# Performance work log

Hardware: AMD Instinct MI355X
Metric: run time of the kernel (lower is better)

The kernel has to match this reference:

```python
import jax, jax.numpy as jnp
import numpy as np

B, S, D, O, E = 8, 4096, 1024, 1024, 64

def setup_inputs() -> dict:
    key = jax.random.key(0)
    kx, kgw, kgb, kew, keb = jax.random.split(key, 5)
    x = jax.random.normal(kx, (B, S, D), dtype=jnp.float32)
    gate_w = jax.random.normal(kgw, (E, D), dtype=jnp.float32) * 0.02
    gate_b = jnp.zeros((E,), dtype=jnp.float32)
    expert_w = jax.random.normal(kew, (E, D, O), dtype=jnp.float32) * 0.02
    expert_b = jnp.zeros((E, O), dtype=jnp.float32)
    return {"x": x, "gate_w": gate_w, "gate_b": gate_b,
            "expert_w": expert_w, "expert_b": expert_b}

def reference(x, gate_w, gate_b, expert_w, expert_b):
    # x: [B,S,D] -> flatten tokens. With world_size=1 the all-reduce and
    # all-to-alls in the torch module are identities, and per-chunk processing
    # is token-independent, so one global pass is mathematically identical.
    b, s, d = x.shape
    xt = x.reshape(-1, d)                                   # [N, D]
    logits = xt @ gate_w.T + gate_b                         # [N, E]
    gates = jax.nn.softmax(logits, axis=-1)
    sel = jnp.argmax(gates, axis=-1)                        # [N] top-1 expert
    order = jnp.argsort(sel)                                # stable sort by expert
    xs = xt[order]                                          # tokens grouped by expert
    counts = jnp.bincount(sel, length=E).astype(jnp.int32)  # tokens per expert
    # Grouped expert GEMM: row block e of xs multiplies expert_w[e].
    ys = jax.lax.ragged_dot(xs, expert_w, counts)           # [N, O]
    ys = ys + expert_b[sel[order]]
    # Combine: scatter sorted outputs back to original token positions.
    # (Note: torch output is NOT scaled by gate probability.)
    out = jnp.zeros((xt.shape[0], expert_w.shape[-1]), dtype=ys.dtype)
    out = out.at[order].set(ys)
    return out.reshape(b, s, -1)
```

## Files before the change

kernel.cpp:

```cpp
#include <hip/hip_runtime.h>
#include <hip/hip_bf16.h>

#define N_TOK 32768
#define DIM 1024
#define OUTD 1024
#define NEXP 64

typedef __attribute__((ext_vector_type(4))) float f32x4;
typedef __attribute__((ext_vector_type(8))) short bf16x8;

__device__ __forceinline__ unsigned short f2bf(float f) {
    unsigned int u = __builtin_bit_cast(unsigned int, f);
    u += 0x7FFFu + ((u >> 16) & 1u);
    return (unsigned short)(u >> 16);
}

#define GLOAD16(gp, lp) \
    __builtin_amdgcn_global_load_lds((const __attribute__((address_space(1))) void*)(gp), \
                                     (__attribute__((address_space(3))) void*)(lp), 16, 0, 0)

__global__ __launch_bounds__(256) void prep_kernel(const float* __restrict__ x,
        const float* __restrict__ gw, const float* __restrict__ gb,
        const float* __restrict__ ew,
        int* __restrict__ sel, int* __restrict__ nflag, int* __restrict__ flags,
        int* __restrict__ counts,
        unsigned short* __restrict__ xb, unsigned short* __restrict__ wt)
{
    __shared__ __align__(16) char smem[18688];
    int tid = threadIdx.x;

    if (blockIdx.x < 512) {
        float (*xs)[36]  = (float(*)[36])smem;
        float (*wsm)[36] = (float(*)[36])(smem + 9216);
        int* h = (int*)(smem + 18432);
        if (tid < NEXP) h[tid] = 0;
        int t0 = blockIdx.x * 64;
        int tg = tid >> 4, eg = tid & 15;

        float acc[4][4];
#pragma unroll
        for (int i = 0; i < 4; i++)
#pragma unroll
            for (int j = 0; j < 4; j++) acc[i][j] = 0.f;

        for (int k0 = 0; k0 < DIM; k0 += 32) {
            __syncthreads();
#pragma unroll
            for (int q = 0; q < 2; q++) {
                int cidx = tid + q * 256;
                int r = cidx >> 3, c4 = (cidx & 7) * 4;
                *reinterpret_cast<float4*>(&xs[r][c4]) =
                    *reinterpret_cast<const float4*>(&x[(size_t)(t0 + r) * DIM + k0 + c4]);
                *reinterpret_cast<float4*>(&wsm[r][c4]) =
                    *reinterpret_cast<const float4*>(&gw[(size_t)r * DIM + k0 + c4]);
            }
            __syncthreads();
            if (xb) {
                int r = tid >> 2, cc = (tid & 3) * 8;
                float4 v0 = *reinterpret_cast<const float4*>(&xs[r][cc]);
                float4 v1 = *reinterpret_cast<const float4*>(&xs[r][cc + 4]);
                uint4 p;
                p.x = (unsigned int)f2bf(v0.x) | ((unsigned int)f2bf(v0.y) << 16);
                p.y = (unsigned int)f2bf(v0.z) | ((unsigned int)f2bf(v0.w) << 16);
                p.z = (unsigned int)f2bf(v1.x) | ((unsigned int)f2bf(v1.y) << 16);
                p.w = (unsigned int)f2bf(v1.z) | ((unsigned int)f2bf(v1.w) << 16);
                *reinterpret_cast<uint4*>(&xb[(size_t)(t0 + r) * DIM + k0 + cc]) = p;
            }
#pragma unroll
            for (int kk4 = 0; kk4 < 8; kk4++) {
                float4 xv[4], wv[4];
#pragma unroll
                for (int i = 0; i < 4; i++)
                    xv[i] = *reinterpret_cast<const float4*>(&xs[tg + 16 * i][kk4 * 4]);
#pragma unroll
                for (int j = 0; j < 4; j++)
                    wv[j] = *reinterpret_cast<const float4*>(&wsm[eg + 16 * j][kk4 * 4]);
#pragma unroll
                for (int i = 0; i < 4; i++)
#pragma unroll
                    for (int j = 0; j < 4; j++) {
                        acc[i][j] = fmaf(xv[i].x, wv[j].x, acc[i][j]);
                        acc[i][j] = fmaf(xv[i].y, wv[j].y, acc[i][j]);
                        acc[i][j] = fmaf(xv[i].z, wv[j].z, acc[i][j]);
                        acc[i][j] = fmaf(xv[i].w, wv[j].w, acc[i][j]);
                    }
            }
        }
#pragma unroll
        for (int j = 0; j < 4; j++) {
            float b = gb[eg + 16 * j];
#pragma unroll
            for (int i = 0; i < 4; i++) acc[i][j] += b;
        }
#pragma unroll
        for (int i = 0; i < 4; i++) {
            float m1 = -1e30f, m2 = -1e30f; int e1 = 0;
#pragma unroll
            for (int j = 0; j < 4; j++) {
                float v = acc[i][j]; int e = eg + 16 * j;
                if (v > m1) { m2 = m1; m1 = v; e1 = e; }
                else if (v > m2) m2 = v;
            }
#pragma unroll
            for (int d = 1; d < 16; d <<= 1) {
                float om1 = __shfl_xor(m1, d, 16);
                float om2 = __shfl_xor(m2, d, 16);
                int   oe1 = __shfl_xor(e1, d, 16);
                if (om1 > m1 || (om1 == m1 && oe1 < e1)) {
                    m2 = fmaxf(om2, m1); m1 = om1; e1 = oe1;
                } else {
                    m2 = fmaxf(m2, om1);
                }
            }
            if (eg == 0) {
                int t = t0 + tg + 16 * i;
                sel[t] = e1;
                atomicAdd(&h[e1], 1);
                if (m1 - m2 < 1e-3f) {
                    int idx = atomicAdd(nflag, 1);
                    if (idx < 4096) flags[idx] = t;
                }
            }
        }
        __syncthreads();
        if (tid < NEXP && h[tid]) atomicAdd(&counts[tid], h[tid]);
    } else {
        if (!wt) return;
        unsigned short* ts0 = (unsigned short*)smem;
        unsigned short* ts1 = (unsigned short*)(smem + 9216);
        int lin = blockIdx.x - 512;
        int e = lin >> 5;
        int d0 = ((lin >> 4) & 1) * 512;
        int o0 = (lin & 15) * 64;
        const float* src = ew + (size_t)e * (DIM * OUTD);
        unsigned short* dst = wt + (size_t)e * (DIM * OUTD);
        int og = tid & 7;
        int dl = tid >> 3;
        int dc = tid & 7;
        int ol = tid >> 3;

        float4 c0, c1, c2, c3;
        {
            const float* sr0 = &src[(size_t)(d0 + dl) * OUTD + o0 + og * 8];
            const float* sr1 = &src[(size_t)(d0 + dl + 32) * OUTD + o0 + og * 8];
            c0 = *reinterpret_cast<const float4*>(sr0);
            c1 = *reinterpret_cast<const float4*>(sr0 + 4);
            c2 = *reinterpret_cast<const float4*>(sr1);
            c3 = *reinterpret_cast<const float4*>(sr1 + 4);
        }
#pragma unroll
        for (int s = 0; s < 8; ++s) {
            float4 n0 = c0, n1 = c1, n2 = c2, n3 = c3;
            if (s < 7) {
                int dsn = d0 + (s + 1) * 64;
                const float* sr0 = &src[(size_t)(dsn + dl) * OUTD + o0 + og * 8];
                const float* sr1 = &src[(size_t)(dsn + dl + 32) * OUTD + o0 + og * 8];
                n0 = *reinterpret_cast<const float4*>(sr0);
                n1 = *reinterpret_cast<const float4*>(sr0 + 4);
                n2 = *reinterpret_cast<const float4*>(sr1);
                n3 = *reinterpret_cast<const float4*>(sr1 + 4);
            }
            unsigned short* tsb = (s & 1) ? ts1 : ts0;
#pragma unroll
            for (int half = 0; half < 2; ++half) {
                int dLoc = dl + 32 * half;
                float4 va = half ? c2 : c0;
                float4 vb = half ? c3 : c1;
                unsigned short b[8] = { f2bf(va.x), f2bf(va.y), f2bf(va.z), f2bf(va.w),
                                        f2bf(vb.x), f2bf(vb.y), f2bf(vb.z), f2bf(vb.w) };
                int dg = dLoc >> 3, dr = dLoc & 7;
#pragma unroll
                for (int k = 0; k < 8; k++) {
                    int o = og * 8 + k;
                    int key = (o & 7) ^ ((o >> 3) & 7);
                    tsb[o * 72 + ((dg ^ key) << 3) + dr] = b[k];
                }
            }
            __syncthreads();
            int ds0 = d0 + s * 64;
#pragma unroll
            for (int i = 0; i < 2; i++) {
                int o = ol + 32 * i;
                int key = (o & 7) ^ ((o >> 3) & 7);
                uint4 v = *reinterpret_cast<const uint4*>(&tsb[o * 72 + ((dc ^ key) << 3)]);
                *reinterpret_cast<uint4*>(&dst[(size_t)(o0 + o) * DIM + ds0 + dc * 8]) = v;
            }
            c0 = n0; c1 = n1; c2 = n2; c3 = n3;
        }
    }
}

__global__ __launch_bounds__(64) void gate_fix_kernel(const float* __restrict__ x,
        const float* __restrict__ gw, const float* __restrict__ gb,
        int* __restrict__ sel, const int* __restrict__ nflag, const int* __restrict__ flags,
        int* __restrict__ counts)
{
    int n = *nflag; if (n > 4096) n = 4096;
    int b = blockIdx.x;
    if (b >= n) return;
    int t = flags[b];
    int e = threadIdx.x;
    const float* xr = x + (size_t)t * DIM;
    const float* wr = gw + (size_t)e * DIM;
    double acc = (double)gb[e];
    for (int k = 0; k < DIM; k += 4) {
        acc += (double)xr[k]   * (double)wr[k];
        acc += (double)xr[k+1] * (double)wr[k+1];
        acc += (double)xr[k+2] * (double)wr[k+2];
        acc += (double)xr[k+3] * (double)wr[k+3];
    }
    double m1 = acc; int e1 = e;
#pragma unroll
    for (int d = 1; d < 64; d <<= 1) {
        double om1 = __shfl_xor(m1, d, 64);
        int   oe1  = __shfl_xor(e1, d, 64);
        if (om1 > m1 || (om1 == m1 && oe1 < e1)) { m1 = om1; e1 = oe1; }
    }
    if (e == 0) {
        int eOld = sel[t];
        if (eOld != e1) {
            sel[t] = e1;
            atomicSub(&counts[eOld], 1);
            atomicAdd(&counts[e1], 1);
        }
    }
}

__global__ void sched_kernel(const int* __restrict__ counts, int* __restrict__ offsets,
                             int* __restrict__ schedE, int* __restrict__ schedR,
                             int* __restrict__ totalRB, int rowsShift)
{
    int e = threadIdx.x;
    int c = counts[e];
    int v = c;
#pragma unroll
    for (int d = 1; d < 64; d <<= 1) { int y = __shfl_up(v, d, 64); if (e >= d) v += y; }
    offsets[e] = v - c;
    if (e == 63) offsets[NEXP] = v;
    int rows = 1 << rowsShift;
    int nb = (c + rows - 1) >> rowsShift;
    int rbv = nb;
#pragma unroll
    for (int d = 1; d < 64; d <<= 1) { int y = __shfl_up(rbv, d, 64); if (e >= d) rbv += y; }
    int rbBase = rbv - nb;
    for (int i = 0; i < nb; i++) { schedE[rbBase + i] = e; schedR[rbBase + i] = i << rowsShift; }
    if (e == 63) *totalRB = rbv;
}

__global__ __launch_bounds__(256) void scatter_kernel(const int* __restrict__ sel,
        const int* __restrict__ offsets, int* __restrict__ cursor, int* __restrict__ perm)
{
    int t = blockIdx.x * 256 + threadIdx.x;
    int e = sel[t];
    int pos = offsets[e] + atomicAdd(&cursor[e], 1);
    perm[pos] = t;
}

__global__ __launch_bounds__(512, 4) void moe_gemm7(
        const unsigned short* __restrict__ xb, const unsigned short* __restrict__ wt,
        const float* __restrict__ eb,
        const int* __restrict__ perm, const int* __restrict__ offsets,
        const int* __restrict__ counts, const int* __restrict__ schedE,
        const int* __restrict__ schedR, const int* __restrict__ totalRB,
        float* __restrict__ out)
{
    int idx = blockIdx.x;
    int xcd = idx & 7;
    int s = idx >> 3;
    int cb = s & 7;
    int rb = (s >> 3) * 8 + xcd;
    if (rb >= *totalRB) return;
    int e = schedE[rb], r0 = schedR[rb];
    int cnt = counts[e], base = offsets[e];

    __shared__ __align__(16) unsigned short As[24576];
    __shared__ __align__(16) unsigned short Bs[12288];

    int tid = threadIdx.x;
    int lane = tid & 63;
    int wv = tid >> 6;
    int wr = wv >> 1, wc = wv & 1;
    int lr = lane & 15, lg = lane >> 4;

    int rowS = tid >> 2;
    int koff = ((tid & 3) ^ ((tid >> 3) & 3)) * 8;
    int rA1 = r0 + rowS, rA2 = r0 + 128 + rowS;
    int tokA1 = (rA1 < cnt) ? perm[base + rA1] : 0;
    int tokA2 = (rA2 < cnt) ? perm[base + rA2] : 0;

    const unsigned short* wte = wt + ((size_t)e << 20);
    const unsigned short* aSrc1 = xb + (size_t)tokA1 * DIM + koff;
    const unsigned short* aSrc2 = xb + (size_t)tokA2 * DIM + koff;
    const unsigned short* bSrc1 = wte + (size_t)(cb * 128 + rowS) * DIM + koff;

    unsigned short* AsQ0 = As + wv * 512;
    unsigned short* AsQ1 = As + 4096 + wv * 512;
    unsigned short* BsQ0 = Bs + wv * 512;

    f32x4 acc[4][4];
#pragma unroll
    for (int m = 0; m < 4; m++)
#pragma unroll
        for (int n = 0; n < 4; n++)
#pragma unroll
            for (int c = 0; c < 4; c++) acc[m][n][c] = 0.f;

    const char* Asc = (const char*)As;
    const char* Bsc = (const char*)Bs;
    int fko = (lg ^ ((lr >> 1) & 3)) * 16;

    auto stage = [&](int buf, int k0) {
        GLOAD16(aSrc1 + k0, AsQ0 + buf * 8192);
        GLOAD16(aSrc2 + k0, AsQ1 + buf * 8192);
        GLOAD16(bSrc1 + k0, BsQ0 + buf * 4096);
    };
    auto compute = [&](int buf) {
        int aoff = buf * 16384;
        int boff = buf * 8192;
        bf16x8 bfr[4];
#pragma unroll
        for (int n = 0; n < 4; n++) {
            int row = wc * 64 + n * 16 + lr;
            bfr[n] = *reinterpret_cast<const bf16x8*>(Bsc + boff + (row << 6) + fko);
        }
        __builtin_amdgcn_s_setprio(1);
#pragma unroll
        for (int m = 0; m < 4; m++) {
            int row = wr * 64 + m * 16 + lr;
            bf16x8 afr = *reinterpret_cast<const bf16x8*>(Asc + aoff + (row << 6) + fko);
#pragma unroll
            for (int n = 0; n < 4; n++)
                acc[m][n] = __builtin_amdgcn_mfma_f32_16x16x32_bf16(afr, bfr[n], acc[m][n], 0, 0, 0);
        }
        __builtin_amdgcn_s_setprio(0);
    };

    stage(0, 0);
    stage(1, 32);

    int cbuf = 0, sbuf = 2;
#pragma unroll 1
    for (int t = 0; t < 30; ++t) {
        asm volatile("s_waitcnt vmcnt(3)" ::: "memory");
        __builtin_amdgcn_s_barrier();
        stage(sbuf, (t + 2) * 32);
        compute(cbuf);
        cbuf = (cbuf == 2) ? 0 : cbuf + 1;
        sbuf = (sbuf == 2) ? 0 : sbuf + 1;
    }
    asm volatile("s_waitcnt vmcnt(3)" ::: "memory");
    __builtin_amdgcn_s_barrier();
    compute(cbuf);
    cbuf = (cbuf == 2) ? 0 : cbuf + 1;
    asm volatile("s_waitcnt vmcnt(0)" ::: "memory");
    __builtin_amdgcn_s_barrier();
    compute(cbuf);

    float bias[4];
#pragma unroll
    for (int n = 0; n < 4; n++)
        bias[n] = eb[e * OUTD + cb * 128 + wc * 64 + n * 16 + lr];
#pragma unroll
    for (int m = 0; m < 4; m++) {
        int rowLoc = wr * 64 + m * 16 + lg * 4;
#pragma unroll
        for (int i2 = 0; i2 < 4; i2++) {
            int r = r0 + rowLoc + i2;
            if (r < cnt) {
                int tk = perm[base + r];
#pragma unroll
                for (int n = 0; n < 4; n++) {
                    int oc = cb * 128 + wc * 64 + n * 16 + lr;
                    out[(size_t)tk * OUTD + oc] = acc[m][n][i2] + bias[n];
                }
            }
        }
    }
}

__global__ __launch_bounds__(256) void moe_gemm_legacy(const float* __restrict__ x,
        const float* __restrict__ ew, const float* __restrict__ eb,
        const int* __restrict__ perm, const int* __restrict__ offsets,
        const int* __restrict__ counts, const int* __restrict__ schedE,
        const int* __restrict__ schedR, const int* __restrict__ totalRB,
        float* __restrict__ out)
{
    int rb = blockIdx.x;
    if (rb >= *totalRB) return;
    int cb = blockIdx.y;
    int e = schedE[rb], r0 = schedR[rb];
    int cnt = counts[e], base = offsets[e];

    __shared__ __align__(16) unsigned short As[128][40];
    __shared__ __align__(16) unsigned short Bs[128][40];
    __shared__ int toks[128];

    int tid = threadIdx.x;
    if (tid < 128) {
        int r = r0 + tid;
        toks[tid] = (r < cnt) ? perm[base + r] : -1;
    }
    __syncthreads();

    int lane = tid & 63;
    int wave = tid >> 6;
    int wr = wave >> 1, wc = wave & 1;
    int lr = lane & 15, lg = lane >> 4;

    f32x4 acc[4][4];
#pragma unroll
    for (int m = 0; m < 4; m++)
#pragma unroll
        for (int n = 0; n < 4; n++)
#pragma unroll
            for (int c = 0; c < 4; c++) acc[m][n][c] = 0.f;

    int aRow[4]; int aTok[4];
#pragma unroll
    for (int q = 0; q < 4; q++) {
        aRow[q] = (tid >> 3) + q * 32;
        int tk = toks[aRow[q]];
        aTok[q] = (tk < 0) ? 0 : tk;
    }
    int ac4 = tid & 7;
    int d0 = (tid >> 5) * 4;
    int o_lane = tid & 31;
    const float* wb = ew + (size_t)e * (DIM * OUTD) + (size_t)cb * 128;

    for (int k0 = 0; k0 < DIM; k0 += 32) {
        float4 av[4];
#pragma unroll
        for (int q = 0; q < 4; q++)
            av[q] = *reinterpret_cast<const float4*>(&x[(size_t)aTok[q] * DIM + k0 + ac4 * 4]);
        float bv[4][4];
#pragma unroll
        for (int i2 = 0; i2 < 4; i2++)
#pragma unroll
            for (int j = 0; j < 4; j++)
                bv[i2][j] = wb[(size_t)(k0 + d0 + i2) * OUTD + o_lane + 32 * j];

        __syncthreads();
#pragma unroll
        for (int q = 0; q < 4; q++) {
            uint2 p;
            p.x = (unsigned int)f2bf(av[q].x) | ((unsigned int)f2bf(av[q].y) << 16);
            p.y = (unsigned int)f2bf(av[q].z) | ((unsigned int)f2bf(av[q].w) << 16);
            *reinterpret_cast<uint2*>(&As[aRow[q]][ac4 * 4]) = p;
        }
#pragma unroll
        for (int j = 0; j < 4; j++) {
            uint2 p;
            p.x = (unsigned int)f2bf(bv[0][j]) | ((unsigned int)f2bf(bv[1][j]) << 16);
            p.y = (unsigned int)f2bf(bv[2][j]) | ((unsigned int)f2bf(bv[3][j]) << 16);
            *reinterpret_cast<uint2*>(&Bs[o_lane + 32 * j][d0]) = p;
        }
        __syncthreads();

        bf16x8 bfr[4];
#pragma unroll
        for (int n = 0; n < 4; n++)
            bfr[n] = *reinterpret_cast<const bf16x8*>(&Bs[wc * 64 + n * 16 + lr][lg * 8]);
#pragma unroll
        for (int m = 0; m < 4; m++) {
            bf16x8 afr = *reinterpret_cast<const bf16x8*>(&As[wr * 64 + m * 16 + lr][lg * 8]);
#pragma unroll
            for (int n = 0; n < 4; n++)
                acc[m][n] = __builtin_amdgcn_mfma_f32_16x16x32_bf16(afr, bfr[n], acc[m][n], 0, 0, 0);
        }
    }

#pragma unroll
    for (int n = 0; n < 4; n++) {
        int oc = cb * 128 + wc * 64 + n * 16 + lr;
        float bias = eb[e * OUTD + oc];
#pragma unroll
        for (int m = 0; m < 4; m++) {
#pragma unroll
            for (int i2 = 0; i2 < 4; i2++) {
                int rr = wr * 64 + m * 16 + lg * 4 + i2;
                int tk = toks[rr];
                if (tk >= 0)
                    out[(size_t)tk * OUTD + oc] = acc[m][n][i2] + bias;
            }
        }
    }
}

extern "C" void kernel_launch(void* const* d_in, const int* in_sizes, int n_in,
                              void* d_out, int out_size, void* d_ws, size_t ws_size,
                              hipStream_t stream)
{
    const float* x  = (const float*)d_in[0];
    const float* gw = (const float*)d_in[1];
    const float* gb = (const float*)d_in[2];
    const float* ew = (const float*)d_in[3];
    const float* eb = (const float*)d_in[4];
    float* out = (float*)d_out;

    char* ws = (char*)d_ws;
    int* counts  = (int*)(ws + 0);
    int* cursor  = (int*)(ws + 256);
    int* offsets = (int*)(ws + 512);
    int* totalRB = (int*)(ws + 1024);
    int* nflag   = (int*)(ws + 1028);
    int* flags   = (int*)(ws + 1032);
    int* schedE  = (int*)(ws + 20480);
    int* schedR  = (int*)(ws + 22528);
    int* sel     = (int*)(ws + 24576);
    int* perm    = (int*)(ws + 155648);

    const size_t WT_OFF   = (size_t)1 << 20;
    const size_t WT_BYTES = (size_t)NEXP * DIM * OUTD * 2;
    const size_t XB_OFF   = WT_OFF + WT_BYTES;
    const size_t XB_BYTES = (size_t)N_TOK * DIM * 2;
    int mode = (ws_size >= XB_OFF + XB_BYTES) ? 2 : 0;
    unsigned short* wt = (mode == 2) ? (unsigned short*)(ws + WT_OFF) : nullptr;
    unsigned short* xb = (mode == 2) ? (unsigned short*)(ws + XB_OFF) : nullptr;

    hipMemsetAsync(ws, 0, 2048, stream);

    prep_kernel<<<dim3(512 + ((mode == 2) ? 2048 : 0)), 256, 0, stream>>>(
        x, gw, gb, ew, sel, nflag, flags, counts, xb, wt);
    gate_fix_kernel<<<dim3(4096), 64, 0, stream>>>(x, gw, gb, sel, nflag, flags, counts);
    sched_kernel<<<dim3(1), 64, 0, stream>>>(counts, offsets, schedE, schedR, totalRB,
                                             (mode == 2) ? 8 : 7);
    scatter_kernel<<<dim3(N_TOK / 256), 256, 0, stream>>>(sel, offsets, cursor, perm);

    if (mode == 2)
        moe_gemm7<<<dim3(1536), 512, 0, stream>>>(xb, wt, eb, perm, offsets, counts,
                                                  schedE, schedR, totalRB, out);
    else
        moe_gemm_legacy<<<dim3(320, 8), 256, 0, stream>>>(x, ew, eb, perm, offsets, counts,
                                                          schedE, schedR, totalRB, out);
}
```

Measured before the change: 382.7 us.

## Compute gating logits with bf16 MFMA and widen near-tie fallback in fp64

The gating GEMM in prep_kernel now uses bf16 MFMA 16x16x32 instructions instead of scalar fp32 FMAs. It also double-buffers the LDS stages, overlaps the next global loads with compute, and uses a swizzled layout. Because bf16 logits are less precise, the near-tie threshold rises from 1e-3 to 0.01 and the flag capacity from 4096 to 16384. This means more tokens get recomputed in fp64 by gate_fix_kernel, which now launches 16384 blocks, and the workspace offsets are rearranged to fit the larger flag array.

```diff
diff --git a/kernel.cpp b/kernel.cpp
--- a/kernel.cpp
+++ b/kernel.cpp
@@ -13,6 +13,15 @@
     unsigned int u = __builtin_bit_cast(unsigned int, f);
     u += 0x7FFFu + ((u >> 16) & 1u);
     return (unsigned short)(u >> 16);
+}
+
+__device__ __forceinline__ uint4 pack8(float4 a, float4 b) {
+    uint4 p;
+    p.x = (unsigned int)f2bf(a.x) | ((unsigned int)f2bf(a.y) << 16);
+    p.y = (unsigned int)f2bf(a.z) | ((unsigned int)f2bf(a.w) << 16);
+    p.z = (unsigned int)f2bf(b.x) | ((unsigned int)f2bf(b.y) << 16);
+    p.w = (unsigned int)f2bf(b.z) | ((unsigned int)f2bf(b.w) << 16);
+    return p;
 }
 
 #define GLOAD16(gp, lp) \
@@ -30,75 +39,80 @@
     int tid = threadIdx.x;
 
     if (blockIdx.x < 512) {
-        float (*xs)[36]  = (float(*)[36])smem;
-        float (*wsm)[36] = (float(*)[36])(smem + 9216);
-        int* h = (int*)(smem + 18432);
+        unsigned short* Ag = (unsigned short*)smem;
+        unsigned short* Bg = (unsigned short*)(smem + 8192);
+        int* h = (int*)(smem + 16384);
         if (tid < NEXP) h[tid] = 0;
+
         int t0 = blockIdx.x * 64;
-        int tg = tid >> 4, eg = tid & 15;
-
-        float acc[4][4];
-#pragma unroll
-        for (int i = 0; i < 4; i++)
-#pragma unroll
-            for (int j = 0; j < 4; j++) acc[i][j] = 0.f;
-
-        for (int k0 = 0; k0 < DIM; k0 += 32) {
+        int lane = tid & 63;
+        int w = tid >> 6;
+        int lr = lane & 15, lg = lane >> 4;
+
+        int rowS = tid >> 2;
+        int koffS = (((tid & 3) ^ ((tid >> 3) & 3)) * 8);
+        const float* xsrc = x + (size_t)(t0 + rowS) * DIM + koffS;
+        const float* wsrc = gw + (size_t)rowS * DIM + koffS;
+        unsigned short* xdst = xb ? xb + (size_t)(t0 + rowS) * DIM + koffS : nullptr;
+
+        f32x4 acc[4];
+#pragma unroll
+        for (int n = 0; n < 4; n++)
+#pragma unroll
+            for (int c = 0; c < 4; c++) acc[n][c] = 0.f;
+
+        float4 v0 = *reinterpret_cast<const float4*>(xsrc);
+        float4 v1 = *reinterpret_cast<const float4*>(xsrc + 4);
+        float4 v2 = *reinterpret_cast<const float4*>(wsrc);
+        float4 v3 = *reinterpret_cast<const float4*>(wsrc + 4);
+        {
+            uint4 pa = pack8(v0, v1), pb = pack8(v2, v3);
+            *reinterpret_cast<uint4*>(&Ag[tid * 8]) = pa;
+            *reinterpret_cast<uint4*>(&Bg[tid * 8]) = pb;
+            if (xdst) *reinterpret_cast<uint4*>(xdst) = pa;
+        }
+        __syncthreads();
+
+        const char* Agc = (const char*)Ag;
+        const char* Bgc = (const char*)Bg;
+        int fko = (lg ^ ((lr >> 1) & 3)) * 16;
+
+#pragma unroll 1
+        for (int t = 0; t < 32; ++t) {
+            if (t < 31) {
+                int k0 = (t + 1) * 32;
+                v0 = *reinterpret_cast<const float4*>(xsrc + k0);
+                v1 = *reinterpret_cast<const float4*>(xsrc + k0 + 4);
+                v2 = *reinterpret_cast<const float4*>(wsrc + k0);
+                v3 = *reinterpret_cast<const float4*>(wsrc + k0 + 4);
+            }
+            int boff = (t & 1) * 4096;
+            bf16x8 afr = *reinterpret_cast<const bf16x8*>(Agc + boff + ((w * 16 + lr) << 6) + fko);
+#pragma unroll
+            for (int n = 0; n < 4; n++) {
+                bf16x8 bfr = *reinterpret_cast<const bf16x8*>(Bgc + boff + ((n * 16 + lr) << 6) + fko);
+                acc[n] = __builtin_amdgcn_mfma_f32_16x16x32_bf16(afr, bfr, acc[n], 0, 0, 0);
+            }
+            if (t < 31) {
+                uint4 pa = pack8(v0, v1), pb = pack8(v2, v3);
+                int soff = ((t + 1) & 1) * 2048;
+                *reinterpret_cast<uint4*>(&Ag[soff + tid * 8]) = pa;
+                *reinterpret_cast<uint4*>(&Bg[soff + tid * 8]) = pb;
+                if (xdst) *reinterpret_cast<uint4*>(xdst + (t + 1) * 32) = pa;
+            }
             __syncthreads();
-#pragma unroll
-            for (int q = 0; q < 2; q++) {
-                int cidx = tid + q * 256;
-                int r = cidx >> 3, c4 = (cidx & 7) * 4;
-                *reinterpret_cast<float4*>(&xs[r][c4]) =
-                    *reinterpret_cast<const float4*>(&x[(size_t)(t0 + r) * DIM + k0 + c4]);
-                *reinterpret_cast<float4*>(&wsm[r][c4]) =
-                    *reinterpret_cast<const float4*>(&gw[(size_t)r * DIM + k0 + c4]);
-            }
-            __syncthreads();
-            if (xb) {
-                int r = tid >> 2, cc = (tid & 3) * 8;
-                float4 v0 = *reinterpret_cast<const float4*>(&xs[r][cc]);
-                float4 v1 = *reinterpret_cast<const float4*>(&xs[r][cc + 4]);
-                uint4 p;
-                p.x = (unsigned int)f2bf(v0.x) | ((unsigned int)f2bf(v0.y) << 16);
-                p.y = (unsigned int)f2bf(v0.z) | ((unsigned int)f2bf(v0.w) << 16);
-                p.z = (unsigned int)f2bf(v1.x) | ((unsigned int)f2bf(v1.y) << 16);
-                p.w = (unsigned int)f2bf(v1.z) | ((unsigned int)f2bf(v1.w) << 16);
-                *reinterpret_cast<uint4*>(&xb[(size_t)(t0 + r) * DIM + k0 + cc]) = p;
-            }
-#pragma unroll
-            for (int kk4 = 0; kk4 < 8; kk4++) {
-                float4 xv[4], wv[4];
-#pragma unroll
-                for (int i = 0; i < 4; i++)
-                    xv[i] = *reinterpret_cast<const float4*>(&xs[tg + 16 * i][kk4 * 4]);
-#pragma unroll
-                for (int j = 0; j < 4; j++)
-                    wv[j] = *reinterpret_cast<const float4*>(&wsm[eg + 16 * j][kk4 * 4]);
-#pragma unroll
-                for (int i = 0; i < 4; i++)
-#pragma unroll
-                    for (int j = 0; j < 4; j++) {
-                        acc[i][j] = fmaf(xv[i].x, wv[j].x, acc[i][j]);
-                        acc[i][j] = fmaf(xv[i].y, wv[j].y, acc[i][j]);
-                        acc[i][j] = fmaf(xv[i].z, wv[j].z, acc[i][j]);
-                        acc[i][j] = fmaf(xv[i].w, wv[j].w, acc[i][j]);
-                    }
-            }
-        }
-#pragma unroll
-        for (int j = 0; j < 4; j++) {
-            float b = gb[eg + 16 * j];
-#pragma unroll
-            for (int i = 0; i < 4; i++) acc[i][j] += b;
-        }
+        }
+
+        float gbv[4];
+#pragma unroll
+        for (int n = 0; n < 4; n++) gbv[n] = gb[n * 16 + lr];
 #pragma unroll
         for (int i = 0; i < 4; i++) {
             float m1 = -1e30f, m2 = -1e30f; int e1 = 0;
 #pragma unroll
-            for (int j = 0; j < 4; j++) {
-                float v = acc[i][j]; int e = eg + 16 * j;
-                if (v > m1) { m2 = m1; m1 = v; e1 = e; }
+            for (int n = 0; n < 4; n++) {
+                float v = acc[n][i] + gbv[n];
+                if (v > m1) { m2 = m1; m1 = v; e1 = n * 16 + lr; }
                 else if (v > m2) m2 = v;
             }
 #pragma unroll
@@ -112,13 +126,13 @@
                     m2 = fmaxf(m2, om1);
                 }
             }
-            if (eg == 0) {
-                int t = t0 + tg + 16 * i;
+            if (lr == 0) {
+                int t = t0 + w * 16 + lg * 4 + i;
                 sel[t] = e1;
                 atomicAdd(&h[e1], 1);
-                if (m1 - m2 < 1e-3f) {
+                if (m1 - m2 < 0.01f) {
                     int idx = atomicAdd(nflag, 1);
-                    if (idx < 4096) flags[idx] = t;
+                    if (idx < 16384) flags[idx] = t;
                 }
             }
         }
@@ -195,7 +209,7 @@
         int* __restrict__ sel, const int* __restrict__ nflag, const int* __restrict__ flags,
         int* __restrict__ counts)
 {
-    int n = *nflag; if (n > 4096) n = 4096;
+    int n = *nflag; if (n > 16384) n = 16384;
     int b = blockIdx.x;
     if (b >= n) return;
     int t = flags[b];
@@ -503,11 +517,11 @@
     int* offsets = (int*)(ws + 512);
     int* totalRB = (int*)(ws + 1024);
     int* nflag   = (int*)(ws + 1028);
-    int* flags   = (int*)(ws + 1032);
-    int* schedE  = (int*)(ws + 20480);
-    int* schedR  = (int*)(ws + 22528);
-    int* sel     = (int*)(ws + 24576);
-    int* perm    = (int*)(ws + 155648);
+    int* schedE  = (int*)(ws + 2048);
+    int* schedR  = (int*)(ws + 4096);
+    int* flags   = (int*)(ws + 8192);
+    int* sel     = (int*)(ws + 131072);
+    int* perm    = (int*)(ws + 262144);
 
     const size_t WT_OFF   = (size_t)1 << 20;
     const size_t WT_BYTES = (size_t)NEXP * DIM * OUTD * 2;
@@ -521,7 +535,7 @@
 
     prep_kernel<<<dim3(512 + ((mode == 2) ? 2048 : 0)), 256, 0, stream>>>(
         x, gw, gb, ew, sel, nflag, flags, counts, xb, wt);
-    gate_fix_kernel<<<dim3(4096), 64, 0, stream>>>(x, gw, gb, sel, nflag, flags, counts);
+    gate_fix_kernel<<<dim3(16384), 64, 0, stream>>>(x, gw, gb, sel, nflag, flags, counts);
     sched_kernel<<<dim3(1), 64, 0, stream>>>(counts, offsets, schedE, schedR, totalRB,
                                              (mode == 2) ? 8 : 7);
     scatter_kernel<<<dim3(N_TOK / 256), 256, 0, stream>>>(sel, offsets, cursor, perm);
```

Result: no change. 377.4 us (-1.4%).
